# Optimization experiments

Hardware: AMD Instinct MI355X
Metric: run time of the kernel (lower is better)

## Reference

```python
import jax, jax.numpy as jnp
import numpy as np
from jax import lax

KS = 3      # generated depthwise kernel size
F = 9       # utils.FILTERS (channels)
P = 24      # utils.PSZ (patch size); conv stride 8 -> KS = P/8


def _extract_patches(x, p):
    # TF extract_patches with sizes=strides=p, VALID: (B,H,W,C) -> (B,nh,nw,p*p*C)
    B, H, W, C = x.shape
    nh, nw = H // p, W // p
    return (x.reshape(B, nh, p, nw, p, C)
             .transpose(0, 1, 3, 2, 4, 5)
             .reshape(B, nh, nw, p * p * C))


def setup_inputs() -> dict:
    key = jax.random.key(0)
    ks = jax.random.split(key, 6)
    B, H, Wd = 16, 384, 384
    return {
        "guidance": jax.random.normal(ks[0], (B, H, Wd, F), jnp.float32),
        "depth": jax.random.normal(ks[1], (B, H, Wd, F), jnp.float32),
        "conv_w": jax.random.normal(ks[2], (KS, KS, F, 9), jnp.float32) * 0.05,
        "conv_b": jax.random.normal(ks[3], (9,), jnp.float32) * 0.05,
        "dense_w": jax.random.normal(ks[4], (F, F * F), jnp.float32) * 0.05,
        "dense_b": jax.random.normal(ks[5], (F * F,), jnp.float32) * 0.05,
    }


def _forward(guidance, depth, conv_w, conv_b, dense_w, dense_b):
    B, H, W, _ = guidance.shape
    NP = (H // P) * (W // P)
    NB = NP * B
    # raw TF reshape (B,nh,nw,P*P*F) -> (NP,B,P,P,F), reproduced faithfully
    gp = _extract_patches(guidance, P).reshape(NP, B, P, P, F)
    dp = _extract_patches(depth, P).reshape(NP, B, P, P, F)

    # --- KGL: per-patch kernel generation (vectorized over NP*B) ---
    gflat = gp.reshape(NB, P, P, F)
    c = lax.conv_general_dilated(gflat, conv_w, (8, 8), 'SAME',
                                 dimension_numbers=('NHWC', 'HWIO', 'NHWC')) + conv_b
    W_G1 = c.reshape(NP, B, KS, KS, F, 1)
    n1 = jnp.sqrt(jnp.sum(W_G1 * W_G1, axis=(2, 3), keepdims=True))
    W_G1 = W_G1 / jnp.maximum(n1, 1.0)          # tf.clip_by_norm(.., 1, axes=[1,2])

    gap = gp.mean(axis=(2, 3))                   # (NP,B,F)
    d = gap @ dense_w + dense_b                  # (NP,B,F*F)
    W_G2 = d.reshape(NP, B, 1, 1, F, F)
    n2 = jnp.sqrt(jnp.sum(W_G2 * W_G2, axis=(2, 3, 4), keepdims=True))
    W_G2 = W_G2 / jnp.maximum(n2, 1.0)           # clip_by_norm axes=[1,2,3]

    # --- per-sample dynamic depthwise conv (vmap over NP*B) ---
    dw_rhs = W_G1.reshape(NB, KS, KS, F, 1).transpose(0, 1, 2, 4, 3)  # HWIO, groups=F
    dflat = dp.reshape(NB, P, P, F)

    def dwconv(img, f):
        return lax.conv_general_dilated(img[None], f, (1, 1), 'SAME',
                                        dimension_numbers=('NHWC', 'HWIO', 'NHWC'),
                                        feature_group_count=F)[0]

    dc = jax.vmap(dwconv)(dflat, dw_rhs)         # (NB,P,P,F)

    # --- per-sample dynamic 1x1 cross-channel conv == matmul ---
    cc = jnp.einsum('npqi,nio->npqo', dc, W_G2.reshape(NB, F, F))
    # raw TF reshape (NP,B,P,P,F) -> (B,H,W,F), reproduced faithfully
    return cc.reshape(B, H, W, F)


def reference(guidance, depth, conv_w, conv_b, dense_w, dense_b):
    return _forward(guidance, depth, conv_w, conv_b, dense_w, dense_b)
```

## Files before the change

kernel.cpp:

```cpp
#include <hip/hip_runtime.h>
#include <stdint.h>


__global__ __launch_bounds__(256) void kgl_kernel(
    const float* __restrict__ g,
    const float* __restrict__ cw,
    const float* __restrict__ cb,
    const float* __restrict__ dw,
    const float* __restrict__ db,
    float* __restrict__ ws)
{
    __shared__ __align__(16) float sg[5184];
    __shared__ float cwf[729];
    __shared__ float cbf[9];
    __shared__ float dwf[729];
    __shared__ float dbf[81];
    __shared__ float cols[216];
    __shared__ float gapm[9];
    __shared__ float cful[81];
    __shared__ float dld[81];

    const int m = blockIdx.x;
    const int t = threadIdx.x;
    const int b0 = m >> 8, pi = (m >> 4) & 15, pj = m & 15;
    const long rowbase = ((long)(b0 * 384 + pi * 24)) * 3456 + (long)pj * 216;

    for (int task = t; task < 1296; task += 256) {
        int r = task / 54, c = task - r * 54;
        const float4* p = reinterpret_cast<const float4*>(g + rowbase + (long)r * 3456);
        reinterpret_cast<float4*>(sg + r * 216)[c] = p[c];
    }
    for (int idx = t; idx < 729; idx += 256) cwf[idx] = cw[idx];
    for (int idx = t; idx < 729; idx += 256) dwf[idx] = dw[idx];
    if (t < 9) cbf[t] = cb[t];
    if (t >= 32 && t < 113) dbf[t - 32] = db[t - 32];
    if (t < 216 && (t % 12) >= 9) ws[(long)m * 216 + t] = 0.0f;
    __syncthreads();

    if (t < 216) {
        float s = 0.f;
        #pragma unroll
        for (int r = 0; r < 24; ++r) s += sg[r * 216 + t];
        cols[t] = s;
    }
    __syncthreads();

    if (t < 81) {
        int o = t % 9, uv = t / 9, v = uv % 3, u = uv / 3;
        float acc = cbf[o];
        #pragma unroll
        for (int du = 0; du < 3; ++du)
        #pragma unroll
        for (int dv = 0; dv < 3; ++dv) {
            const float* gp2 = &sg[(u * 8 + du) * 216 + (v * 8 + dv) * 9];
            const float* wp  = &cwf[(du * 3 + dv) * 81 + o];
            #pragma unroll
            for (int ci = 0; ci < 9; ++ci) acc += gp2[ci] * wp[ci * 9];
        }
        cful[t] = acc;
    }
    if (t >= 216 && t < 225) {
        int f = t - 216; float s = 0.f;
        #pragma unroll
        for (int c = 0; c < 24; ++c) s += cols[c * 9 + f];
        gapm[f] = s * (1.0f / 576.0f);
    }
    __syncthreads();

    if (t < 81) {
        float acc = dbf[t];
        #pragma unroll
        for (int k = 0; k < 9; ++k) acc += gapm[k] * dwf[k * 81 + t];
        dld[t] = acc;
    }
    if (t >= 96 && t < 105) {
        int f = t - 96; float s = 0.f;
        #pragma unroll
        for (int k = 0; k < 9; ++k) { float c = cful[k * 9 + f]; s += c * c; }
        float scale = (s > 1.0f) ? (1.0f / sqrtf(s)) : 1.0f;
        float* wout = ws + (long)m * 216;
        #pragma unroll
        for (int k = 0; k < 9; ++k) wout[k * 12 + f] = cful[k * 9 + f] * scale;
    }
    __syncthreads();

    if (t < 9) {
        float s = 0.f;
        #pragma unroll
        for (int i = 0; i < 9; ++i) { float d = dld[i * 9 + t]; s += d * d; }
        float scale = (s > 1.0f) ? (1.0f / sqrtf(s)) : 1.0f;
        float* wout = ws + (long)m * 216 + 108;
        #pragma unroll
        for (int i = 0; i < 9; ++i) wout[t * 12 + i] = dld[i * 9 + t] * scale;
    }
}

__global__ __launch_bounds__(256) void apply_kernel(
    const float* __restrict__ dep,
    const float* __restrict__ ws,
    float* __restrict__ out)
{
    __shared__ __align__(16) float sd[8112];
    __shared__ float sw[216];
    __shared__ __align__(16) float ob[5184];

    const int m = blockIdx.x;
    const int t = threadIdx.x;
    const int b0 = m >> 8, pi = (m >> 4) & 15, pj = m & 15;
    const long rowbase = ((long)(b0 * 384 + pi * 24)) * 3456 + (long)pj * 216;

    for (int e = t; e < 8112; e += 256) sd[e] = 0.0f;
    if (t < 216) sw[t] = ws[(long)m * 216 + t];
    __syncthreads();

    for (int task = t; task < 1296; task += 256) {
        int r = task / 54, c4 = task - r * 54;
        const float4* p = reinterpret_cast<const float4*>(dep + rowbase + (long)r * 3456);
        float4 v = p[c4];
        float vv[4] = { v.x, v.y, v.z, v.w };
        int e0 = c4 * 4;
        #pragma unroll
        for (int s = 0; s < 4; ++s) {
            int e = e0 + s;
            int col = e / 9, f = e - col * 9;
            sd[((r + 1) * 26 + (col + 1)) * 12 + f] = vv[s];
        }
    }
    __syncthreads();

    if (t < 192) {
        const int row = t >> 3;
        const int qb = (t & 7) * 3;
        float dc[3][9];
        #pragma unroll
        for (int k = 0; k < 3; ++k)
            #pragma unroll
            for (int i = 0; i < 9; ++i) dc[k][i] = 0.f;

        #pragma unroll
        for (int du = 0; du < 3; ++du) {
            float nb[5][9];
            #pragma unroll
            for (int c = 0; c < 5; ++c) {
                const float* sp = &sd[((row + du) * 26 + qb + c) * 12];
                float4 A = *reinterpret_cast<const float4*>(sp);
                float4 B = *reinterpret_cast<const float4*>(sp + 4);
                nb[c][0] = A.x; nb[c][1] = A.y; nb[c][2] = A.z; nb[c][3] = A.w;
                nb[c][4] = B.x; nb[c][5] = B.y; nb[c][6] = B.z; nb[c][7] = B.w;
                nb[c][8] = sp[8];
            }
            #pragma unroll
            for (int dv = 0; dv < 3; ++dv) {
                const float* wv = &sw[(du * 3 + dv) * 12];
                #pragma unroll
                for (int i = 0; i < 9; ++i) {
                    float w = wv[i];
                    dc[0][i] += nb[dv][i]     * w;
                    dc[1][i] += nb[dv + 1][i] * w;
                    dc[2][i] += nb[dv + 2][i] * w;
                }
            }
        }
        float* op = &ob[(row * 24 + qb) * 9];
        #pragma unroll
        for (int o = 0; o < 9; ++o) {
            const float* wv = &sw[108 + o * 12];
            float a0 = 0.f, a1 = 0.f, a2 = 0.f;
            #pragma unroll
            for (int i = 0; i < 9; ++i) {
                float w = wv[i];
                a0 += dc[0][i] * w; a1 += dc[1][i] * w; a2 += dc[2][i] * w;
            }
            op[o]      = a0;
            op[9 + o]  = a1;
            op[18 + o] = a2;
        }
    }
    __syncthreads();

    {
        const float4* src = reinterpret_cast<const float4*>(ob);
        float4* dst = reinterpret_cast<float4*>(out) + (long)m * 1296;
        for (int k = t; k < 1296; k += 256) dst[k] = src[k];
    }
}

extern "C" void kernel_launch(void* const* d_in, const int* in_sizes, int n_in,
                              void* d_out, int out_size, void* d_ws, size_t ws_size,
                              hipStream_t stream) {
    const float* g  = (const float*)d_in[0];
    const float* dp = (const float*)d_in[1];
    const float* cw = (const float*)d_in[2];
    const float* cb = (const float*)d_in[3];
    const float* dw = (const float*)d_in[4];
    const float* db = (const float*)d_in[5];
    float* ws = (float*)d_ws;
    float* out = (float*)d_out;

    kgl_kernel<<<dim3(4096), dim3(256), 0, stream>>>(g, cw, cb, dw, db, ws);
    apply_kernel<<<dim3(4096), dim3(256), 0, stream>>>(dp, ws, out);
}
```

Before: 271.1 us.

## Use one thread per output pixel in apply kernel and drop output staging

```diff
diff --git a/kernel.cpp b/kernel.cpp
--- a/kernel.cpp
+++ b/kernel.cpp
@@ -95,25 +95,31 @@
     }
 }
 
-__global__ __launch_bounds__(256) void apply_kernel(
+__global__ __launch_bounds__(576, 7) void apply_kernel(
     const float* __restrict__ dep,
     const float* __restrict__ ws,
     float* __restrict__ out)
 {
     __shared__ __align__(16) float sd[8112];
     __shared__ float sw[216];
-    __shared__ __align__(16) float ob[5184];
 
     const int m = blockIdx.x;
     const int t = threadIdx.x;
     const int b0 = m >> 8, pi = (m >> 4) & 15, pj = m & 15;
     const long rowbase = ((long)(b0 * 384 + pi * 24)) * 3456 + (long)pj * 216;
 
-    for (int e = t; e < 8112; e += 256) sd[e] = 0.0f;
-    if (t < 216) sw[t] = ws[(long)m * 216 + t];
-    __syncthreads();
-
-    for (int task = t; task < 1296; task += 256) {
+    if (t < 100) {
+        int r, c;
+        if (t < 26)      { r = 0;       c = t;      }
+        else if (t < 52) { r = 25;      c = t - 26; }
+        else if (t < 76) { r = t - 51;  c = 0;      }
+        else             { r = t - 75;  c = 25;     }
+        float4 z = make_float4(0.f, 0.f, 0.f, 0.f);
+        float4* p = reinterpret_cast<float4*>(&sd[(r * 26 + c) * 12]);
+        p[0] = z; p[1] = z; p[2] = z;
+    }
+    if (t >= 128 && t < 344) sw[t - 128] = ws[(long)m * 216 + (t - 128)];
+    for (int task = t; task < 1296; task += 576) {
         int r = task / 54, c4 = task - r * 54;
         const float4* p = reinterpret_cast<const float4*>(dep + rowbase + (long)r * 3456);
         float4 v = p[c4];
@@ -128,60 +134,36 @@
     }
     __syncthreads();
 
-    if (t < 192) {
-        const int row = t >> 3;
-        const int qb = (t & 7) * 3;
-        float dc[3][9];
+    {
+        const int row = t / 24;
+        const int col = t - row * 24;
+        float dc[9];
         #pragma unroll
-        for (int k = 0; k < 3; ++k)
-            #pragma unroll
-            for (int i = 0; i < 9; ++i) dc[k][i] = 0.f;
+        for (int i = 0; i < 9; ++i) dc[i] = 0.f;
 
         #pragma unroll
-        for (int du = 0; du < 3; ++du) {
-            float nb[5][9];
-            #pragma unroll
-            for (int c = 0; c < 5; ++c) {
-                const float* sp = &sd[((row + du) * 26 + qb + c) * 12];
-                float4 A = *reinterpret_cast<const float4*>(sp);
-                float4 B = *reinterpret_cast<const float4*>(sp + 4);
-                nb[c][0] = A.x; nb[c][1] = A.y; nb[c][2] = A.z; nb[c][3] = A.w;
-                nb[c][4] = B.x; nb[c][5] = B.y; nb[c][6] = B.z; nb[c][7] = B.w;
-                nb[c][8] = sp[8];
-            }
-            #pragma unroll
-            for (int dv = 0; dv < 3; ++dv) {
-                const float* wv = &sw[(du * 3 + dv) * 12];
-                #pragma unroll
-                for (int i = 0; i < 9; ++i) {
-                    float w = wv[i];
-                    dc[0][i] += nb[dv][i]     * w;
-                    dc[1][i] += nb[dv + 1][i] * w;
-                    dc[2][i] += nb[dv + 2][i] * w;
-                }
-            }
+        for (int du = 0; du < 3; ++du)
+        #pragma unroll
+        for (int dv = 0; dv < 3; ++dv) {
+            const float* sp = &sd[((row + du) * 26 + (col + dv)) * 12];
+            const float* wv = &sw[(du * 3 + dv) * 12];
+            float4 A = *reinterpret_cast<const float4*>(sp);
+            float4 B = *reinterpret_cast<const float4*>(sp + 4);
+            float a8 = sp[8];
+            dc[0] += A.x * wv[0]; dc[1] += A.y * wv[1]; dc[2] += A.z * wv[2];
+            dc[3] += A.w * wv[3]; dc[4] += B.x * wv[4]; dc[5] += B.y * wv[5];
+            dc[6] += B.z * wv[6]; dc[7] += B.w * wv[7]; dc[8] += a8  * wv[8];
         }
-        float* op = &ob[(row * 24 + qb) * 9];
+
+        float* op = out + (long)m * 5184 + t * 9;
         #pragma unroll
         for (int o = 0; o < 9; ++o) {
             const float* wv = &sw[108 + o * 12];
-            float a0 = 0.f, a1 = 0.f, a2 = 0.f;
+            float a = 0.f;
             #pragma unroll
-            for (int i = 0; i < 9; ++i) {
-                float w = wv[i];
-                a0 += dc[0][i] * w; a1 += dc[1][i] * w; a2 += dc[2][i] * w;
-            }
-            op[o]      = a0;
-            op[9 + o]  = a1;
-            op[18 + o] = a2;
+            for (int i = 0; i < 9; ++i) a += dc[i] * wv[i];
+            op[o] = a;
         }
-    }
-    __syncthreads();
-
-    {
-        const float4* src = reinterpret_cast<const float4*>(ob);
-        float4* dst = reinterpret_cast<float4*>(out) + (long)m * 1296;
-        for (int k = t; k < 1296; k += 256) dst[k] = src[k];
     }
 }
 
@@ -198,5 +180,5 @@
     float* out = (float*)d_out;
 
     kgl_kernel<<<dim3(4096), dim3(256), 0, stream>>>(g, cw, cb, dw, db, ws);
-    apply_kernel<<<dim3(4096), dim3(256), 0, stream>>>(dp, ws, out);
+    apply_kernel<<<dim3(4096), dim3(576), 0, stream>>>(dp, ws, out);
 }
```

Measured after the change: 254.8 us. 6.0% less time.
